# Optimization experiments

Measured on AMD Instinct MI355X. Metric: run time of the kernel, lower is better.

## Reference

```python
import jax, jax.numpy as jnp
import numpy as np

B, M, S, A = 256, 256, 32, 33
NH, NOUT = 3, 100
F_IN = 2 * S + 2          # 66, GAT input features
ALPHA = 0.01              # leaky-relu slope
LN_EPS = 1e-5


def setup_inputs() -> dict:
    key = jax.random.key(0)
    ks = jax.random.split(key, 13)
    obs_dim = 5 * M + 2 + 2 * M * S
    obs = jax.random.normal(ks[0], (B, obs_dim), jnp.float32)
    adj = jax.random.randint(ks[1], (M, M), 0, 2).astype(jnp.int32)
    u_gumbel = jax.random.uniform(ks[2], (B, M, A), jnp.float32)
    W_gat = jax.random.normal(ks[3], (NH, F_IN, NOUT), jnp.float32) * 0.1
    a_gat = jax.random.normal(ks[4], (NH, 2 * NOUT), jnp.float32) * 0.1
    ln_w = jax.random.normal(ks[5], (NH * NOUT,), jnp.float32) * 0.5
    ln_b = jnp.zeros((NH * NOUT,), jnp.float32)
    W1 = jax.random.normal(ks[6], (3 * M + 2, 100), jnp.float32) * 0.05
    b1 = jax.random.normal(ks[7], (100,), jnp.float32) * 0.7
    d2_in = 100 + NH * M * NOUT
    W2 = jax.random.normal(ks[8], (d2_in, 128), jnp.float32) * 0.005
    b2 = jax.random.normal(ks[9], (128,), jnp.float32) * 0.7
    Wout = jax.random.normal(ks[10], (M, 128, A), jnp.float32) * 0.1
    bout = jax.random.normal(ks[11], (M, A), jnp.float32) * 0.7
    return dict(obs=obs, adj=adj, u_gumbel=u_gumbel, W_gat=W_gat, a_gat=a_gat,
                ln_w=ln_w, ln_b=ln_b, W1=W1, b1=b1, W2=W2, b2=b2,
                Wout=Wout, bout=bout)


def _actor_fwd(obs, u_gumbel, W_gat, a_gat, ln_w, ln_b, W1, b1, W2, b2, Wout, bout, adj):
    # --- split obs per Actor.forward slicing ---
    server_state = obs[:, :3 * M + 2]                       # [B, 3m+2]
    mcs_res = obs[:, 3 * M + 2:4 * M + 2].reshape(B, M, 1)
    mcs_ins = obs[:, 4 * M + 2:5 * M + 2].reshape(B, M, 1)
    base = 5 * M + 2
    resp = obs[:, base:base + M * S].reshape(B, M, S)
    insp = obs[:, base + M * S:].reshape(B, M, S)
    feat = jnp.concatenate([mcs_res, mcs_ins, resp, insp], axis=-1)  # [B,M,2s+2]

    # --- GAT layer (eval mode: dropouts are identity) ---
    Wh = jnp.einsum('bmf,hfo->hbmo', feat, W_gat)           # [H,B,M,O]
    # e[b,i,j] = leakyrelu(a1 . Wh_i + a2 . Wh_j)  (same math as the
    # original O(N^2,2f) repeat/cat, expressed without materializing it)
    e1 = jnp.einsum('hbmo,ho->hbm', Wh, a_gat[:, :NOUT])
    e2 = jnp.einsum('hbmo,ho->hbm', Wh, a_gat[:, NOUT:])
    e = jax.nn.leaky_relu(e1[..., :, None] + e2[..., None, :], ALPHA)  # [H,B,M,M]
    e = jnp.where(adj > 0, e, jnp.float32(-9e15))
    att = jax.nn.softmax(e, axis=-2)                        # torch softmax(dim=1)
    h_prime = jax.nn.elu(jnp.einsum('hbij,hbjo->hbio', att, Wh))
    feats = jnp.moveaxis(h_prime, 0, 2).reshape(B, M, NH * NOUT)  # head concat
    mu = jnp.mean(feats, axis=-1, keepdims=True)
    var = jnp.var(feats, axis=-1, keepdims=True)
    gat_out = (feats - mu) * jax.lax.rsqrt(var + LN_EPS) * ln_w + ln_b
    gat_out = jax.nn.elu(gat_out)                           # GAT.forward elu_
    mcs_gat = gat_out.reshape(B, -1)                        # [B, 3*m*100]

    # --- dense heads ---
    server_feat = jax.nn.relu(jax.nn.elu(server_state @ W1 + b1))
    hidden = jax.nn.relu(jax.nn.elu(
        jnp.concatenate([server_feat, mcs_gat], axis=-1) @ W2 + b2))  # [B,128]

    # per-mcs heads, vectorized: logits[b,m,a]
    logits = jnp.tanh(jax.nn.elu(jnp.einsum('bh,mha->bma', hidden, Wout) + bout))

    # gumbel-softmax (tau=1, hard=True, straight-through)
    u = jnp.clip(u_gumbel, 1e-10, 1.0 - 1e-10)
    g = -jnp.log(-jnp.log(u))
    y_soft = jax.nn.softmax(logits + g, axis=-1)
    y_hard = jax.nn.one_hot(jnp.argmax(y_soft, axis=-1), A, dtype=y_soft.dtype)
    actions = y_hard + y_soft - jax.lax.stop_gradient(y_soft)
    return actions.reshape(B, M * A)


def reference(obs, adj, u_gumbel, W_gat, a_gat, ln_w, ln_b, W1, b1, W2, b2, Wout, bout):
    return _actor_fwd(obs, u_gumbel, W_gat, a_gat, ln_w, ln_b, W1, b1, W2, b2, Wout, bout, adj)
```

## Files before the change

### kernel.cpp

```cpp
#include <hip/hip_runtime.h>
#include <math.h>

constexpr int B    = 256;
constexpr int M    = 256;
constexpr int A    = 33;
constexpr int NH   = 3;
constexpr int NO   = 100;
constexpr int FIN  = 66;
constexpr int OBSD = 17666;
constexpr int D1   = 770;
constexpr int D2G  = 76800;

__device__ __forceinline__ float lrelu(float x) { return x > 0.f ? x : 0.01f * x; }
__device__ __forceinline__ float eluf(float x)  { return x > 0.f ? x : expm1f(x); }

__global__ __launch_bounds__(256) void k_adjmask(const int* __restrict__ adj,
                                                 unsigned* __restrict__ adjm) {
  int w = blockIdx.x * 256 + threadIdx.x;
  if (w >= M * 8) return;
  int i = w >> 3, wd = w & 7;
  const int* row = adj + i * M + wd * 32;
  unsigned mval = 0;
  #pragma unroll
  for (int bit = 0; bit < 32; ++bit) mval |= (row[bit] > 0 ? 1u : 0u) << bit;
  adjm[w] = mval;
}

__global__ __launch_bounds__(256) void k_wh(const float* __restrict__ obs,
                                            const float* __restrict__ Wg,
                                            const float* __restrict__ ag,
                                            float* __restrict__ Wh,
                                            float* __restrict__ e1,
                                            float* __restrict__ e2) {
  int b = blockIdx.x, h = blockIdx.y;
  int t = threadIdx.x;
  int to = t >> 4;
  int tm = t & 15;
  __shared__ float smem_w[66 * 104 + 32];
  __shared__ float featT[66 * 132];
  __shared__ float a1s[128], a2s[128];
  const float* ob = obs + (size_t)b * OBSD;

  for (int idx = t; idx < 66 * 104 + 32; idx += 256) {
    float v = 0.f;
    if (idx < 66 * 104) {
      int f = idx / 104, o = idx % 104;
      if (o < NO) v = Wg[((size_t)h * FIN + f) * NO + o];
    }
    smem_w[idx] = v;
  }
  if (t < 128) {
    a1s[t] = (t < NO) ? ag[h * 200 + t] : 0.f;
    a2s[t] = (t < NO) ? ag[h * 200 + NO + t] : 0.f;
  }

  size_t basee = ((size_t)h * B + b) * M;

  for (int tile = 0; tile < 2; ++tile) {
    int m0 = tile * 128;
    if (t < 128)       featT[t]               = ob[770  + m0 + t];
    else               featT[132 + (t - 128)] = ob[1026 + m0 + (t - 128)];
    for (int idx = t; idx < 128 * 32; idx += 256) {
      int m = idx >> 5, s = idx & 31;
      featT[(2  + s) * 132 + m] = ob[1282 + (size_t)(m0 + m) * 32 + s];
      featT[(34 + s) * 132 + m] = ob[9474 + (size_t)(m0 + m) * 32 + s];
    }
    __syncthreads();

    float acc[8][8];
    #pragma unroll
    for (int q = 0; q < 8; ++q)
      #pragma unroll
      for (int p = 0; p < 8; ++p) acc[q][p] = 0.f;

    for (int f = 0; f < 66; ++f) {
      const float* fr = featT + f * 132 + tm * 8;
      const float* wr = smem_w + f * 104 + to * 8;
      float4 fa = *(const float4*)fr;
      float4 fb = *(const float4*)(fr + 4);
      float4 wa = *(const float4*)wr;
      float4 wb = *(const float4*)(wr + 4);
      float fm[8] = {fa.x, fa.y, fa.z, fa.w, fb.x, fb.y, fb.z, fb.w};
      float wv[8] = {wa.x, wa.y, wa.z, wa.w, wb.x, wb.y, wb.z, wb.w};
      #pragma unroll
      for (int q = 0; q < 8; ++q)
        #pragma unroll
        for (int p = 0; p < 8; ++p) acc[q][p] += fm[q] * wv[p];
    }
    __syncthreads();

    float* e1p = featT;
    float* e2p = featT + 128 * 18;
    #pragma unroll
    for (int q = 0; q < 8; ++q) {
      float p1 = 0.f, p2 = 0.f;
      #pragma unroll
      for (int p = 0; p < 8; ++p) {
        float av = acc[q][p];
        p1 += av * a1s[to * 8 + p];
        p2 += av * a2s[to * 8 + p];
      }
      e1p[(tm * 8 + q) * 18 + to] = p1;
      e2p[(tm * 8 + q) * 18 + to] = p2;
    }

    #pragma unroll
    for (int q = 0; q < 8; ++q) {
      int m = m0 + tm * 8 + q;
      float* wp = Wh + (basee + m) * NO + to * 8;
      if (to <= 12) *(float4*)wp       = make_float4(acc[q][0], acc[q][1], acc[q][2], acc[q][3]);
      if (to <= 11) *(float4*)(wp + 4) = make_float4(acc[q][4], acc[q][5], acc[q][6], acc[q][7]);
    }
    __syncthreads();

    if (t < 128) {
      float s1 = 0.f, s2 = 0.f;
      #pragma unroll
      for (int u = 0; u < 16; ++u) {
        s1 += e1p[t * 18 + u];
        s2 += e2p[t * 18 + u];
      }
      e1[basee + m0 + t] = s1;
      e2[basee + m0 + t] = s2;
    }
    __syncthreads();
  }
}

__global__ __launch_bounds__(256) void k_colstats(const float* __restrict__ e1,
                                                  const float* __restrict__ e2,
                                                  const unsigned* __restrict__ adjm,
                                                  float* __restrict__ cmax,
                                                  float* __restrict__ csum) {
  int b = blockIdx.x, h = blockIdx.y, j = threadIdx.x;
  __shared__ float e1s[M];
  __shared__ unsigned ams[M * 8];
  size_t base = ((size_t)h * B + b) * M;
  e1s[j] = e1[base + j];
  for (int w = j; w < M * 8; w += 256) ams[w] = adjm[w];
  __syncthreads();
  float e2j = e2[base + j];
  int jw = j >> 5;
  unsigned jb = 1u << (j & 31);
  float mx = -INFINITY;
  for (int i = 0; i < M; ++i) {
    float v = (ams[i * 8 + jw] & jb) ? lrelu(e1s[i] + e2j) : -9e15f;
    mx = fmaxf(mx, v);
  }
  float sm = 0.f;
  for (int i = 0; i < M; ++i) {
    float v = (ams[i * 8 + jw] & jb) ? lrelu(e1s[i] + e2j) : -9e15f;
    sm += expf(v - mx);
  }
  cmax[base + j] = mx;
  csum[base + j] = sm;
}

__global__ __launch_bounds__(256) void k_attn(const float* __restrict__ Wh,
                                              const float* __restrict__ e1,
                                              const float* __restrict__ e2,
                                              const float* __restrict__ cmax,
                                              const float* __restrict__ csum,
                                              const unsigned* __restrict__ adjm,
                                              float* __restrict__ feats) {
  int b = blockIdx.x, h = blockIdx.y, os = blockIdx.z;
  int t = threadIdx.x;
  int o0 = os * 50;
  __shared__ float WhT[128 * 52];
  __shared__ float e2s[M], cms[M], csr[M];
  size_t base = ((size_t)h * B + b) * M;

  e2s[t] = e2[base + t];
  cms[t] = cmax[base + t];
  csr[t] = 1.0f / csum[base + t];

  unsigned mrow[8];
  #pragma unroll
  for (int w = 0; w < 8; ++w) mrow[w] = adjm[t * 8 + w];
  float ei = e1[base + t];

  float acc[52];
  #pragma unroll
  for (int q = 0; q < 52; ++q) acc[q] = 0.f;

  const float* WhG = Wh + base * NO;
  for (int jh = 0; jh < 2; ++jh) {
    __syncthreads();
    const float* src = WhG + (size_t)jh * 128 * NO + o0;
    for (int idx = t; idx < 128 * 52; idx += 256) {
      int jj = idx / 52, o = idx - jj * 52;
      WhT[idx] = (o < 50) ? src[(size_t)jj * NO + o] : 0.f;
    }
    __syncthreads();
    for (int jj = 0; jj < 128; ++jj) {
      int j = jh * 128 + jj;
      unsigned bit = (mrow[j >> 5] >> (j & 31)) & 1u;
      float v = bit ? lrelu(ei + e2s[j]) : -9e15f;
      float p = expf(v - cms[j]) * csr[j];
      const float4* w4 = (const float4*)(WhT + jj * 52);
      #pragma unroll
      for (int q = 0; q < 13; ++q) {
        float4 wv = w4[q];
        acc[4*q+0] += p * wv.x;
        acc[4*q+1] += p * wv.y;
        acc[4*q+2] += p * wv.z;
        acc[4*q+3] += p * wv.w;
      }
    }
  }

  for (int chunk = 0; chunk < 2; ++chunk) {
    __syncthreads();
    if ((t >> 7) == chunk) {
      float* dst = WhT + (t & 127) * 52;
      #pragma unroll
      for (int q = 0; q < 50; ++q) dst[q] = acc[q];
    }
    __syncthreads();
    for (int idx = t; idx < 128 * 50; idx += 256) {
      int r = idx / 50, o = idx - r * 50;
      feats[((size_t)b * M + chunk * 128 + r) * 300 + h * NO + o0 + o] =
          eluf(WhT[r * 52 + o]);
    }
  }
}

__global__ __launch_bounds__(256) void k_lnstats(const float* __restrict__ g,
                                                 float* __restrict__ mu_out,
                                                 float* __restrict__ rs_out) {
  int gid = blockIdx.x * 256 + threadIdx.x;
  int wid = gid >> 6, lane = gid & 63;
  const float* row = g + (size_t)wid * 300;
  float v[5];
  float s = 0.f;
  #pragma unroll
  for (int j = 0; j < 5; ++j) {
    int i = j * 64 + lane;
    v[j] = (i < 300) ? row[i] : 0.f;
    s += v[j];
  }
  #pragma unroll
  for (int d = 1; d < 64; d <<= 1) s += __shfl_xor(s, d);
  float mu = s * (1.f / 300.f);
  float ss = 0.f;
  #pragma unroll
  for (int j = 0; j < 5; ++j) {
    int i = j * 64 + lane;
    float dd = (i < 300) ? (v[j] - mu) : 0.f;
    ss += dd * dd;
  }
  #pragma unroll
  for (int d = 1; d < 64; d <<= 1) ss += __shfl_xor(ss, d);
  if (lane == 0) {
    mu_out[wid] = mu;
    rs_out[wid] = 1.0f / sqrtf(ss * (1.f / 300.f) + 1e-5f);
  }
}

__global__ __launch_bounds__(256) void k_sf(const float* __restrict__ obs,
                                            const float* __restrict__ W1,
                                            const float* __restrict__ b1,
                                            float* __restrict__ sf) {
  int b = blockIdx.x, t = threadIdx.x;
  int k = t & 127, fc = t >> 7;
  __shared__ float ss[D1];
  __shared__ float red[256];
  const float* ob = obs + (size_t)b * OBSD;
  for (int i = t; i < D1; i += 256) ss[i] = ob[i];
  __syncthreads();
  float acc = 0.f;
  if (k < NO) {
    int f0 = fc * 385;
    #pragma unroll 8
    for (int f = f0; f < f0 + 385; ++f) acc += ss[f] * W1[(size_t)f * NO + k];
  }
  red[t] = acc;
  __syncthreads();
  if (t < 128 && k < NO) {
    float v = red[t] + red[t + 128] + b1[k];
    sf[b * NO + k] = fmaxf(eluf(v), 0.f);
  }
}

__global__ __launch_bounds__(256) void k_gemm2(const float* __restrict__ gat,
                                               const float* __restrict__ mu,
                                               const float* __restrict__ rs,
                                               const float* __restrict__ lw,
                                               const float* __restrict__ lb,
                                               const float* __restrict__ W2,
                                               float* __restrict__ pre) {
  int bt = blockIdx.x, dc = blockIdx.y;
  int t = threadIdx.x;
  int k = t & 127, g2 = t >> 7;
  __shared__ float gt[16 * 124];
  int b0 = bt * 16, d0 = dc * 1200;
  float acc[8];
  #pragma unroll
  for (int r = 0; r < 8; ++r) acc[r] = 0.f;
  for (int ds0 = 0; ds0 < 1200; ds0 += 120) {
    int dsg = d0 + ds0;
    __syncthreads();
    for (int idx = t; idx < 16 * 120; idx += 256) {
      int rr = idx / 120, cc = idx - rr * 120;
      int gidx = dsg + cc;
      int brow = b0 + rr;
      int mrow = gidx / 300;
      int d    = gidx - mrow * 300;
      int lrow = brow * M + mrow;
      float x = gat[(size_t)brow * D2G + gidx];
      float val = (x - mu[lrow]) * rs[lrow] * lw[d] + lb[d];
      gt[rr * 124 + cc] = eluf(val);
    }
    __syncthreads();
    const float* w2p = W2 + (size_t)(100 + dsg) * 128 + k;
    for (int c4 = 0; c4 < 30; ++c4) {
      float w0  = w2p[(size_t)(c4 * 4 + 0) * 128];
      float w1  = w2p[(size_t)(c4 * 4 + 1) * 128];
      float w2v = w2p[(size_t)(c4 * 4 + 2) * 128];
      float w3  = w2p[(size_t)(c4 * 4 + 3) * 128];
      #pragma unroll
      for (int r = 0; r < 8; ++r) {
        float4 gv = *(const float4*)(gt + (g2 * 8 + r) * 124 + c4 * 4);
        acc[r] += gv.x * w0 + gv.y * w1 + gv.z * w2v + gv.w * w3;
      }
    }
  }
  #pragma unroll
  for (int r = 0; r < 8; ++r)
    pre[((size_t)dc * B + b0 + g2 * 8 + r) * 128 + k] = acc[r];
}

__global__ __launch_bounds__(256) void k_hid(const float* __restrict__ pre,
                                             const float* __restrict__ sf,
                                             const float* __restrict__ W2,
                                             const float* __restrict__ b2,
                                             float* __restrict__ hid,
                                             float* __restrict__ hidT) {
  int b = blockIdx.x, t = threadIdx.x;
  int k = t & 127, p = t >> 7;
  __shared__ float red[256];
  float s = 0.f;
  const float* sfb = sf + b * NO;
  #pragma unroll 4
  for (int dc = p * 32; dc < p * 32 + 32; ++dc)
    s += pre[((size_t)dc * B + b) * 128 + k];
  #pragma unroll 4
  for (int f = p * 50; f < p * 50 + 50; ++f)
    s += sfb[f] * W2[(size_t)f * 128 + k];
  red[t] = s;
  __syncthreads();
  if (t < 128) {
    float v = red[t] + red[t + 128] + b2[k];
    v = fmaxf(eluf(v), 0.f);
    hid[(size_t)b * 128 + k] = v;
    hidT[(size_t)k * B + b]  = v;
  }
}

__global__ __launch_bounds__(256) void k_out(const float* __restrict__ hidT,
                                             const float* __restrict__ Wout,
                                             const float* __restrict__ bout,
                                             const float* __restrict__ ug,
                                             float* __restrict__ out) {
  int m = blockIdx.x, b = threadIdx.x;
  __shared__ float wo[128 * 36];
  for (int idx = b; idx < 128 * 36; idx += 256) {
    int kk = idx / 36, a = idx % 36;
    wo[idx] = (a < A) ? Wout[(size_t)m * 128 * A + kk * A + a] : 0.f;
  }
  __syncthreads();
  float l[36];
  #pragma unroll
  for (int a = 0; a < 36; ++a) l[a] = (a < A) ? bout[m * A + a] : 0.f;
  for (int kk = 0; kk < 128; ++kk) {
    float hv = hidT[(size_t)kk * B + b];
    const float4* w4 = (const float4*)(wo + kk * 36);
    #pragma unroll
    for (int q = 0; q < 9; ++q) {
      float4 wv = w4[q];
      l[4*q+0] += hv * wv.x;
      l[4*q+1] += hv * wv.y;
      l[4*q+2] += hv * wv.z;
      l[4*q+3] += hv * wv.w;
    }
  }
  const float* ugp = ug + ((size_t)b * M + m) * A;
  float mx = -INFINITY;
  int amx = 0;
  #pragma unroll
  for (int a = 0; a < A; ++a) {
    float th = tanhf(eluf(l[a]));
    float u = ugp[a];
    u = fminf(fmaxf(u, 1e-10f), 1.0f - 1e-10f);
    float gb = -logf(-logf(u));
    float z = th + gb;
    l[a] = z;
    if (z > mx) { mx = z; amx = a; }
  }
  float sm = 0.f;
  #pragma unroll
  for (int a = 0; a < A; ++a) { float e = expf(l[a] - mx); l[a] = e; sm += e; }
  float* op = out + ((size_t)b * M + m) * A;
  #pragma unroll
  for (int a = 0; a < A; ++a) {
    float ys = l[a] / sm;
    float yh = (a == amx) ? 1.0f : 0.0f;
    op[a] = (yh + ys) - ys;
  }
}

extern "C" void kernel_launch(void* const* d_in, const int* in_sizes, int n_in,
                              void* d_out, int out_size, void* d_ws, size_t ws_size,
                              hipStream_t stream) {
  const float* obs  = (const float*)d_in[0];
  const int*   adj  = (const int*)  d_in[1];
  const float* ug   = (const float*)d_in[2];
  const float* Wg   = (const float*)d_in[3];
  const float* ag   = (const float*)d_in[4];
  const float* lw   = (const float*)d_in[5];
  const float* lb   = (const float*)d_in[6];
  const float* W1   = (const float*)d_in[7];
  const float* b1   = (const float*)d_in[8];
  const float* W2   = (const float*)d_in[9];
  const float* b2   = (const float*)d_in[10];
  const float* Wout = (const float*)d_in[11];
  const float* bout = (const float*)d_in[12];
  float* out = (float*)d_out;

  float* ws = (float*)d_ws;
  size_t off = 0;
  float* Wh    = ws + off; off += (size_t)NH * B * M * NO;
  float* feats = ws + off; off += (size_t)B * M * 300;
  float* e1    = ws + off; off += (size_t)NH * B * M;
  float* e2    = ws + off; off += (size_t)NH * B * M;
  float* cmx   = ws + off; off += (size_t)NH * B * M;
  float* csm   = ws + off; off += (size_t)NH * B * M;
  float* sf    = ws + off; off += (size_t)B * NO;
  float* pre   = ws + off; off += (size_t)64 * B * 128;
  float* hid   = ws + off; off += (size_t)B * 128;
  float* hidT  = ws + off; off += (size_t)B * 128;
  float* muA   = ws + off; off += (size_t)B * M;
  float* rsA   = ws + off; off += (size_t)B * M;
  unsigned* adjm = (unsigned*)(ws + off);

  k_adjmask <<<dim3(8),         256, 0, stream>>>(adj, adjm);
  k_wh      <<<dim3(B, NH),     256, 0, stream>>>(obs, Wg, ag, Wh, e1, e2);
  k_colstats<<<dim3(B, NH),     256, 0, stream>>>(e1, e2, adjm, cmx, csm);
  k_attn    <<<dim3(B, NH, 2),  256, 0, stream>>>(Wh, e1, e2, cmx, csm, adjm, feats);
  k_lnstats <<<dim3(B * M / 4), 256, 0, stream>>>(feats, muA, rsA);
  k_sf      <<<dim3(B),         256, 0, stream>>>(obs, W1, b1, sf);
  k_gemm2   <<<dim3(16, 64),    256, 0, stream>>>(feats, muA, rsA, lw, lb, W2, pre);
  k_hid     <<<dim3(B),         256, 0, stream>>>(pre, sf, W2, b2, hid, hidT);
  k_out     <<<dim3(M),         256, 0, stream>>>(hidT, Wout, bout, ug, out);
}
```

Measured before the change: 801.2 us.

## Fuse column softmax stats into k_wh and register-tile the attention GEMM

```diff
diff --git a/kernel.cpp b/kernel.cpp
--- a/kernel.cpp
+++ b/kernel.cpp
@@ -29,9 +29,12 @@
 __global__ __launch_bounds__(256) void k_wh(const float* __restrict__ obs,
                                             const float* __restrict__ Wg,
                                             const float* __restrict__ ag,
+                                            const unsigned* __restrict__ adjm,
                                             float* __restrict__ Wh,
                                             float* __restrict__ e1,
-                                            float* __restrict__ e2) {
+                                            float* __restrict__ e2,
+                                            float* __restrict__ cmax,
+                                            float* __restrict__ csum) {
   int b = blockIdx.x, h = blockIdx.y;
   int t = threadIdx.x;
   int to = t >> 4;
@@ -39,6 +42,8 @@
   __shared__ float smem_w[66 * 104 + 32];
   __shared__ float featT[66 * 132];
   __shared__ float a1s[128], a2s[128];
+  __shared__ float e1a[256], e2a[256];
+  __shared__ unsigned ams[M * 8];
   const float* ob = obs + (size_t)b * OBSD;
 
   for (int idx = t; idx < 66 * 104 + 32; idx += 256) {
@@ -53,6 +58,7 @@
     a1s[t] = (t < NO) ? ag[h * 200 + t] : 0.f;
     a2s[t] = (t < NO) ? ag[h * 200 + NO + t] : 0.f;
   }
+  for (int w = t; w < M * 8; w += 256) ams[w] = adjm[w];
 
   size_t basee = ((size_t)h * B + b) * M;
 
@@ -122,38 +128,29 @@
       }
       e1[basee + m0 + t] = s1;
       e2[basee + m0 + t] = s2;
-    }
-    __syncthreads();
-  }
-}
-
-__global__ __launch_bounds__(256) void k_colstats(const float* __restrict__ e1,
-                                                  const float* __restrict__ e2,
-                                                  const unsigned* __restrict__ adjm,
-                                                  float* __restrict__ cmax,
-                                                  float* __restrict__ csum) {
-  int b = blockIdx.x, h = blockIdx.y, j = threadIdx.x;
-  __shared__ float e1s[M];
-  __shared__ unsigned ams[M * 8];
-  size_t base = ((size_t)h * B + b) * M;
-  e1s[j] = e1[base + j];
-  for (int w = j; w < M * 8; w += 256) ams[w] = adjm[w];
-  __syncthreads();
-  float e2j = e2[base + j];
-  int jw = j >> 5;
-  unsigned jb = 1u << (j & 31);
-  float mx = -INFINITY;
-  for (int i = 0; i < M; ++i) {
-    float v = (ams[i * 8 + jw] & jb) ? lrelu(e1s[i] + e2j) : -9e15f;
-    mx = fmaxf(mx, v);
-  }
-  float sm = 0.f;
-  for (int i = 0; i < M; ++i) {
-    float v = (ams[i * 8 + jw] & jb) ? lrelu(e1s[i] + e2j) : -9e15f;
-    sm += expf(v - mx);
-  }
-  cmax[base + j] = mx;
-  csum[base + j] = sm;
+      e1a[m0 + t] = s1;
+      e2a[m0 + t] = s2;
+    }
+    __syncthreads();
+  }
+
+  {
+    float e2j = e2a[t];
+    int jw = t >> 5;
+    unsigned jb = 1u << (t & 31);
+    float mx = -INFINITY;
+    for (int i = 0; i < M; ++i) {
+      float v = (ams[i * 8 + jw] & jb) ? lrelu(e1a[i] + e2j) : -9e15f;
+      mx = fmaxf(mx, v);
+    }
+    float sm = 0.f;
+    for (int i = 0; i < M; ++i) {
+      float v = (ams[i * 8 + jw] & jb) ? lrelu(e1a[i] + e2j) : -9e15f;
+      sm += expf(v - mx);
+    }
+    cmax[basee + t] = mx;
+    csum[basee + t] = sm;
+  }
 }
 
 __global__ __launch_bounds__(256) void k_attn(const float* __restrict__ Wh,
@@ -163,64 +160,86 @@
                                               const float* __restrict__ csum,
                                               const unsigned* __restrict__ adjm,
                                               float* __restrict__ feats) {
-  int b = blockIdx.x, h = blockIdx.y, os = blockIdx.z;
+  int b = blockIdx.x, h = blockIdx.y, ih = blockIdx.z;
   int t = threadIdx.x;
-  int o0 = os * 50;
-  __shared__ float WhT[128 * 52];
-  __shared__ float e2s[M], cms[M], csr[M];
+  int to = t & 15, ti = t >> 4;
+  int i0 = ih * 128;
+  __shared__ float WhC[32 * 104];
+  __shared__ float attT[32 * 132];
+  __shared__ float e1s[128];
+  __shared__ float e2s[256], cms[256], csr[256];
+  __shared__ unsigned amsT[8 * 136];
   size_t base = ((size_t)h * B + b) * M;
 
+  if (t < 128) e1s[t] = e1[base + i0 + t];
   e2s[t] = e2[base + t];
   cms[t] = cmax[base + t];
   csr[t] = 1.0f / csum[base + t];
-
-  unsigned mrow[8];
-  #pragma unroll
-  for (int w = 0; w < 8; ++w) mrow[w] = adjm[t * 8 + w];
-  float ei = e1[base + t];
-
-  float acc[52];
-  #pragma unroll
-  for (int q = 0; q < 52; ++q) acc[q] = 0.f;
+  for (int idx = t; idx < 8 * 128; idx += 256) {
+    int w = idx >> 7, il = idx & 127;
+    amsT[w * 136 + il] = adjm[(size_t)(i0 + il) * 8 + w];
+  }
+
+  float acc[8][8];
+  #pragma unroll
+  for (int q = 0; q < 8; ++q)
+    #pragma unroll
+    for (int p = 0; p < 8; ++p) acc[q][p] = 0.f;
 
   const float* WhG = Wh + base * NO;
-  for (int jh = 0; jh < 2; ++jh) {
-    __syncthreads();
-    const float* src = WhG + (size_t)jh * 128 * NO + o0;
-    for (int idx = t; idx < 128 * 52; idx += 256) {
-      int jj = idx / 52, o = idx - jj * 52;
-      WhT[idx] = (o < 50) ? src[(size_t)jj * NO + o] : 0.f;
-    }
-    __syncthreads();
-    for (int jj = 0; jj < 128; ++jj) {
-      int j = jh * 128 + jj;
-      unsigned bit = (mrow[j >> 5] >> (j & 31)) & 1u;
-      float v = bit ? lrelu(ei + e2s[j]) : -9e15f;
-      float p = expf(v - cms[j]) * csr[j];
-      const float4* w4 = (const float4*)(WhT + jj * 52);
-      #pragma unroll
-      for (int q = 0; q < 13; ++q) {
-        float4 wv = w4[q];
-        acc[4*q+0] += p * wv.x;
-        acc[4*q+1] += p * wv.y;
-        acc[4*q+2] += p * wv.z;
-        acc[4*q+3] += p * wv.w;
+  int jp = t >> 3;
+  int iu = (t & 7) * 16;
+
+  for (int c = 0; c < 8; ++c) {
+    __syncthreads();
+    for (int idx = t; idx < 32 * 104; idx += 256) {
+      int r = idx / 104, o = idx - r * 104;
+      WhC[idx] = (o < NO) ? WhG[(size_t)(c * 32 + r) * NO + o] : 0.f;
+    }
+    {
+      int jg = c * 32 + jp;
+      float e2j = e2s[jg], cmj = cms[jg], rsj = csr[jg];
+      unsigned wbit = 1u << (jg & 31);
+      const unsigned* aw = amsT + (jg >> 5) * 136 + iu;
+      const float* ep = e1s + iu;
+      float* ap = attT + jp * 132 + iu;
+      #pragma unroll
+      for (int r = 0; r < 16; ++r) {
+        float v = (aw[r] & wbit) ? lrelu(ep[r] + e2j) : -9e15f;
+        ap[r] = expf(v - cmj) * rsj;
       }
     }
-  }
-
-  for (int chunk = 0; chunk < 2; ++chunk) {
-    __syncthreads();
-    if ((t >> 7) == chunk) {
-      float* dst = WhT + (t & 127) * 52;
-      #pragma unroll
-      for (int q = 0; q < 50; ++q) dst[q] = acc[q];
-    }
-    __syncthreads();
-    for (int idx = t; idx < 128 * 50; idx += 256) {
-      int r = idx / 50, o = idx - r * 50;
-      feats[((size_t)b * M + chunk * 128 + r) * 300 + h * NO + o0 + o] =
-          eluf(WhT[r * 52 + o]);
+    __syncthreads();
+    for (int j = 0; j < 32; ++j) {
+      const float4* a4 = (const float4*)(attT + j * 132 + ti * 8);
+      const float4* w4 = (const float4*)(WhC + j * 104 + to * 8);
+      float4 aa = a4[0], ab = a4[1];
+      float4 wa = w4[0], wb = w4[1];
+      float av[8] = {aa.x, aa.y, aa.z, aa.w, ab.x, ab.y, ab.z, ab.w};
+      float wv[8] = {wa.x, wa.y, wa.z, wa.w, wb.x, wb.y, wb.z, wb.w};
+      #pragma unroll
+      for (int q = 0; q < 8; ++q)
+        #pragma unroll
+        for (int p = 0; p < 8; ++p) acc[q][p] += av[q] * wv[p];
+    }
+  }
+
+  if (to < 13) {
+    #pragma unroll
+    for (int q = 0; q < 8; ++q) {
+      int i = i0 + ti * 8 + q;
+      float* fp = feats + ((size_t)b * M + i) * 300 + h * NO + to * 8;
+      if (to < 12) {
+        float4 v0 = make_float4(eluf(acc[q][0]), eluf(acc[q][1]), eluf(acc[q][2]), eluf(acc[q][3]));
+        float4 v1 = make_float4(eluf(acc[q][4]), eluf(acc[q][5]), eluf(acc[q][6]), eluf(acc[q][7]));
+        *(float4*)fp       = v0;
+        *(float4*)(fp + 4) = v1;
+      } else {
+        fp[0] = eluf(acc[q][0]);
+        fp[1] = eluf(acc[q][1]);
+        fp[2] = eluf(acc[q][2]);
+        fp[3] = eluf(acc[q][3]);
+      }
     }
   }
 }
@@ -444,8 +463,7 @@
   unsigned* adjm = (unsigned*)(ws + off);
 
   k_adjmask <<<dim3(8),         256, 0, stream>>>(adj, adjm);
-  k_wh      <<<dim3(B, NH),     256, 0, stream>>>(obs, Wg, ag, Wh, e1, e2);
-  k_colstats<<<dim3(B, NH),     256, 0, stream>>>(e1, e2, adjm, cmx, csm);
+  k_wh      <<<dim3(B, NH),     256, 0, stream>>>(obs, Wg, ag, adjm, Wh, e1, e2, cmx, csm);
   k_attn    <<<dim3(B, NH, 2),  256, 0, stream>>>(Wh, e1, e2, cmx, csm, adjm, feats);
   k_lnstats <<<dim3(B * M / 4), 256, 0, stream>>>(feats, muA, rsA);
   k_sf      <<<dim3(B),         256, 0, stream>>>(obs, W1, b1, sf);
```

Measured after the change: 798.3 us. Within noise of the previous version (-0.4%).
